# Kernel optimization log

Hardware: AMD Instinct MI355X
Metric: run time of the kernel (lower is better)

## Reference

```python
import jax, jax.numpy as jnp
import numpy as np
from jax.scipy.linalg import cho_solve

N, D, T, K, P = 4000, 256, 52, 20, 100
EPS = 1e-8


def _make_kernel(length_scale):
    # RBF kernel over time grid with the same jitter-doubling rule as the torch code.
    t = np.arange(T, dtype=np.float32)
    sq = (t[None, :] - t[:, None]) ** 2
    Kmat = np.exp(-0.5 * sq / np.float32(length_scale) ** 2).astype(np.float32)
    jitter = 1e-4
    eye = np.eye(T, dtype=np.float32)
    while True:
        if np.linalg.cond(Kmat + jitter * eye) < 1e4:
            break
        jitter *= 2
        if jitter > 0.1:
            break
    return jnp.asarray(Kmat + jitter * eye)

K_LAMBDA = _make_kernel(T / 4)  # lambda GP kernel, shared across all k
K_PHI = _make_kernel(T / 3)     # phi GP kernel, shared across all k


def setup_inputs() -> dict:
    key = jax.random.key(0)
    ks = jax.random.split(key, 7)
    lambda_ = jax.random.normal(ks[0], (N, K, T), dtype=jnp.float32)
    phi = jax.random.normal(ks[1], (K, D, T), dtype=jnp.float32)
    gamma = 0.1 * jax.random.normal(ks[2], (P, K), dtype=jnp.float32)
    G = jax.random.normal(ks[3], (N, P), dtype=jnp.float32)
    Y = (jax.random.uniform(ks[4], (N, D, T)) < 0.05).astype(jnp.float32)
    logit_prev_t = jax.random.normal(ks[5], (D, T), dtype=jnp.float32) - 3.0
    event_times = jax.random.randint(ks[6], (N, D), 0, T)
    return dict(lambda_=lambda_, phi=phi, gamma=gamma, G=G, Y=Y,
                logit_prev_t=logit_prev_t, event_times=event_times)


def reference(lambda_, phi, gamma, G, Y, logit_prev_t, event_times):
    # --- forward: softmax over topics, sigmoid disease probs, mixture ---
    theta = jax.nn.softmax(lambda_, axis=1)          # [N,K,T]
    phi_prob = jax.nn.sigmoid(phi)                   # [K,D,T]
    pi = jnp.einsum('nkt,kdt->ndt', theta, phi_prob) # [N,D,T]
    pi = jnp.clip(pi, EPS, 1.0 - EPS)

    # --- survival data loss ---
    tgrid = jnp.arange(T)[None, None, :]             # [1,1,T]
    e = event_times[:, :, None]                      # [N,D,1]
    mask_before = (tgrid < e).astype(pi.dtype)
    mask_at = (tgrid == e).astype(pi.dtype)
    log_pi = jnp.log(pi)
    log_1mpi = jnp.log1p(-pi)
    loss_censored = -jnp.sum(log_1mpi * mask_before)
    loss_event = -jnp.sum(log_pi * mask_at * Y)
    loss_no_event = -jnp.sum(log_1mpi * mask_at * (1.0 - Y))
    data_loss = (loss_censored + loss_event + loss_no_event) / N

    # --- GP prior loss: batched cholesky solves replace per-sample loops ---
    L_lam = jnp.linalg.cholesky(K_LAMBDA)            # [T,T]
    L_phi = jnp.linalg.cholesky(K_PHI)               # [T,T]
    mean_lam = G @ gamma                             # [N,K]
    dev_lam = (lambda_ - mean_lam[:, :, None]).reshape(N * K, T)  # [N*K,T]
    v_lam = cho_solve((L_lam, True), dev_lam.T)      # [T,N*K]
    gp_lambda = 0.5 * jnp.sum(dev_lam.T * v_lam)
    dev_phi = (phi - logit_prev_t[None, :, :]).reshape(K * D, T)  # [K*D,T]
    v_phi = cho_solve((L_phi, True), dev_phi.T)      # [T,K*D]
    gp_phi = 0.5 * jnp.sum(dev_phi.T * v_phi)
    gp_loss = gp_lambda / N + gp_phi / D

    return data_loss + gp_loss
```

## Files before the change

### kernel.cpp

```cpp
#include <hip/hip_runtime.h>
#include <math.h>
#include <string.h>

#define Nn 4000
#define Dd 256
#define Tt 52
#define Kk 20
#define Pp 100
#define CH 4
#define TC 13

#define OFF_W       0
#define OFF_MLAM_P  5408
#define OFF_MPHI_P  343408
#define OFF_DLP     397488
#define OFF_EVP     399488
#define OFF_PHIP    655488
#define OFF_THETA   921728

#define GR_ROWS 128

#define RB_PHIP0   0
#define RB_THETA0  52
#define RB_GPHI0   865
#define RB_GLAM0   885
#define RB_EVP0    1010
#define RB_TOTAL   1138

__global__ __launch_bounds__(256) void prep_kernel(
    const float* __restrict__ lam, const float* __restrict__ phi,
    const float* __restrict__ gamma, const float* __restrict__ G,
    const float* __restrict__ logit_prev, const int* __restrict__ ev,
    float* __restrict__ theta_t, float* __restrict__ phip_t,
    unsigned char* __restrict__ evp,
    float* __restrict__ Mlam_p, float* __restrict__ Mphi_p) {
    __shared__ float rows[GR_ROWS][56];
    __shared__ float meanv[GR_ROWS];
    const int bx = blockIdx.x, tid = threadIdx.x;

    if (bx < RB_THETA0) {
        int gid = bx * 256 + tid;
        int d = gid / Tt, t = gid - d * Tt;
        float v[Kk];
#pragma unroll
        for (int k = 0; k < Kk; ++k) {
            float x = phi[k * (Dd * Tt) + gid];
            v[k] = 1.f / (1.f + __expf(-x));
        }
#pragma unroll
        for (int k = 0; k < Kk; ++k)
            phip_t[((size_t)t * Kk + k) * Dd + d] = v[k];
        return;
    }
    if (bx < RB_GPHI0) {
        int gid = (bx - RB_THETA0) * 256 + tid;
        if (gid >= Nn * Tt) return;
        int n = gid / Tt, t = gid - n * Tt;
        const float* base = lam + n * Kk * Tt + t;
        float v[Kk];
        float m = -1e30f;
#pragma unroll
        for (int k = 0; k < Kk; ++k) { v[k] = base[k * Tt]; m = fmaxf(m, v[k]); }
        float s = 0.f;
#pragma unroll
        for (int k = 0; k < Kk; ++k) { v[k] = __expf(v[k] - m); s += v[k]; }
        float inv = 1.f / s;
        float* o = theta_t + ((size_t)t * Nn + n) * Kk;
#pragma unroll
        for (int k = 0; k < Kk; ++k) o[k] = v[k] * inv;
        return;
    }
    if (bx < RB_GLAM0) {
        int slot = bx - RB_GPHI0;
        int ta = tid % 13, tb = tid / 13;
        float acc[4][4] = {};
        for (int it = 0; it < 2; ++it) {
            int R0 = (slot * 2 + it) * GR_ROWS;
            __syncthreads();
            for (int idx = tid; idx < GR_ROWS * Tt; idx += 256) {
                int r = idx / Tt, t = idx - r * Tt;
                int R = R0 + r;
                rows[r][t] = phi[R * Tt + t] - logit_prev[(R & 255) * Tt + t];
            }
            __syncthreads();
            if (tb < 13) {
                for (int r = 0; r < GR_ROWS; ++r) {
                    float4 a = *(const float4*)&rows[r][4 * ta];
                    float4 b = *(const float4*)&rows[r][4 * tb];
                    float av[4] = {a.x, a.y, a.z, a.w};
                    float bv[4] = {b.x, b.y, b.z, b.w};
#pragma unroll
                    for (int i = 0; i < 4; ++i)
#pragma unroll
                        for (int j = 0; j < 4; ++j) acc[i][j] += av[i] * bv[j];
                }
            }
        }
        if (tb < 13)
#pragma unroll
            for (int i = 0; i < 4; ++i)
#pragma unroll
                for (int j = 0; j < 4; ++j)
                    Mphi_p[slot * 2704 + (4 * ta + i) * Tt + 4 * tb + j] = acc[i][j];
        return;
    }
    if (bx < RB_EVP0) {
        int slot = bx - RB_GLAM0;
        int ta = tid % 13, tb = tid / 13;
        float acc[4][4] = {};
        for (int it = 0; it < 5; ++it) {
            int R0 = (slot * 5 + it) * GR_ROWS;
            __syncthreads();
            if (tid < GR_ROWS) {
                int R = R0 + tid;
                int n = R / Kk, k = R - n * Kk;
                float m = 0.f;
                for (int p = 0; p < Pp; ++p) m += G[n * Pp + p] * gamma[p * Kk + k];
                meanv[tid] = m;
            }
            __syncthreads();
            for (int idx = tid; idx < GR_ROWS * Tt; idx += 256) {
                int r = idx / Tt, t = idx - r * Tt;
                int R = R0 + r;
                rows[r][t] = lam[R * Tt + t] - meanv[r];
            }
            __syncthreads();
            if (tb < 13) {
                for (int r = 0; r < GR_ROWS; ++r) {
                    float4 a = *(const float4*)&rows[r][4 * ta];
                    float4 b = *(const float4*)&rows[r][4 * tb];
                    float av[4] = {a.x, a.y, a.z, a.w};
                    float bv[4] = {b.x, b.y, b.z, b.w};
#pragma unroll
                    for (int i = 0; i < 4; ++i)
#pragma unroll
                        for (int j = 0; j < 4; ++j) acc[i][j] += av[i] * bv[j];
                }
            }
        }
        if (tb < 13)
#pragma unroll
            for (int i = 0; i < 4; ++i)
#pragma unroll
                for (int j = 0; j < 4; ++j)
                    Mlam_p[slot * 2704 + (4 * ta + i) * Tt + 4 * tb + j] = acc[i][j];
        return;
    }
    {
        const int4* src = (const int4*)ev;
        unsigned int* dst = (unsigned int*)evp;
        int gtid = (bx - RB_EVP0) * 256 + tid;
        for (int i = gtid; i < (Nn * Dd) / 4; i += 128 * 256) {
            int4 v = src[i];
            dst[i] = (unsigned)v.x | ((unsigned)v.y << 8) |
                     ((unsigned)v.z << 16) | ((unsigned)v.w << 24);
        }
        return;
    }
}

__global__ __launch_bounds__(256) void data_kernel(const float* __restrict__ theta_t,
                                                   const float* __restrict__ phip_t,
                                                   const float* __restrict__ Y,
                                                   const unsigned char* __restrict__ evp,
                                                   float* __restrict__ DLp) {
    __shared__ float wsum[4];
    const int tid = threadIdx.x;
    const int d = tid;
    const int ng = blockIdx.x >> 2;
    const int t0 = (blockIdx.x & 3) * TC;
    const int n0 = ng * 8;

    int e[8];
    float Yv[8], acc[8], pie[8], prod[8];
#pragma unroll
    for (int g = 0; g < 8; ++g) {
        e[g] = evp[(n0 + g) * Dd + d];
        acc[g] = 0.f;
        prod[g] = 1.f;
        pie[g] = 0.5f;
        Yv[g] = 0.f;
        if (e[g] >= t0 && e[g] < t0 + TC)
            Yv[g] = __builtin_nontemporal_load(
                Y + ((size_t)((n0 + g) * Dd + d)) * Tt + e[g]);
    }

    for (int j = 0; j < TC; ++j) {
        int t = t0 + j;
        float pv[Kk];
        const float* pt = phip_t + (size_t)t * (Kk * Dd) + d;
#pragma unroll
        for (int k = 0; k < Kk; ++k) pv[k] = pt[k * Dd];
#pragma unroll
        for (int g = 0; g < 8; ++g) {
            const float4* th = (const float4*)(theta_t + ((size_t)t * Nn + n0 + g) * Kk);
            float4 a0 = th[0], a1 = th[1], a2 = th[2], a3 = th[3], a4 = th[4];
            float pi = a0.x * pv[0] + a0.y * pv[1] + a0.z * pv[2] + a0.w * pv[3]
                     + a1.x * pv[4] + a1.y * pv[5] + a1.z * pv[6] + a1.w * pv[7]
                     + a2.x * pv[8] + a2.y * pv[9] + a2.z * pv[10] + a2.w * pv[11]
                     + a3.x * pv[12] + a3.y * pv[13] + a3.z * pv[14] + a3.w * pv[15]
                     + a4.x * pv[16] + a4.y * pv[17] + a4.z * pv[18] + a4.w * pv[19];
            pi = fminf(fmaxf(pi, 1e-8f), 1.0f - 1e-8f);
            prod[g] *= (t <= e[g]) ? (1.f - pi) : 1.f;
            pie[g] = (t == e[g]) ? pi : pie[g];
        }
        if ((j & 3) == 3 || j == TC - 1) {
#pragma unroll
            for (int g = 0; g < 8; ++g) { acc[g] += __logf(prod[g]); prod[g] = 1.f; }
        }
    }
    float tsum = 0.f;
#pragma unroll
    for (int g = 0; g < 8; ++g)
        tsum += acc[g] + Yv[g] * (__logf(pie[g]) - __logf(1.f - pie[g]));
    for (int off = 32; off; off >>= 1) tsum += __shfl_down(tsum, off, 64);
    if ((tid & 63) == 0) wsum[tid >> 6] = tsum;
    __syncthreads();
    if (tid == 0)
        DLp[blockIdx.x] = -(wsum[0] + wsum[1] + wsum[2] + wsum[3]);
}

__global__ __launch_bounds__(1024) void final_kernel(const float* __restrict__ ws,
                                                     float* __restrict__ out) {
    const int tid = threadIdx.x;
    double s = 0.0;
    for (int i = tid; i < 2704; i += 1024) {
        double ml = 0.0, mp = 0.0;
        for (int b = 0; b < 125; ++b) ml += (double)ws[OFF_MLAM_P + b * 2704 + i];
        for (int b = 0; b < 20; ++b)  mp += (double)ws[OFF_MPHI_P + b * 2704 + i];
        s += (double)ws[OFF_W + i] * ml + (double)ws[OFF_W + 2704 + i] * mp;
    }
    double dl = 0.0;
    for (int i = tid; i < (Nn / 8) * CH; i += 1024) dl += (double)ws[OFF_DLP + i];
    s += dl / Nn;
    __shared__ double red[1024];
    red[tid] = s;
    __syncthreads();
    for (int off = 512; off; off >>= 1) {
        if (tid < off) red[tid] += red[tid + off];
        __syncthreads();
    }
    if (tid == 0) out[0] = (float)red[0];
}


static void build_K_f(double ls_in, float Kf[52][52]) {
    float ls = (float)ls_in;
    float ls2 = ls * ls;
    for (int i = 0; i < 52; ++i)
        for (int j = 0; j < 52; ++j) {
            float sq = (float)((i - j) * (i - j));
            float arg = (-0.5f * sq) / ls2;
            Kf[i][j] = expf(arg);
        }
}

static void jacobi_eig(double a[52][52], double ev[52]) {
    const int n = 52;
    for (int sweep = 0; sweep < 100; ++sweep) {
        double off = 0;
        for (int p = 0; p < n - 1; ++p)
            for (int q = p + 1; q < n; ++q) off += a[p][q] * a[p][q];
        if (off < 1e-24) break;
        for (int p = 0; p < n - 1; ++p)
            for (int q = p + 1; q < n; ++q) {
                double apq = a[p][q];
                if (fabs(apq) < 1e-300) continue;
                double th = (a[q][q] - a[p][p]) / (2.0 * apq);
                double t = (th >= 0 ? 1.0 : -1.0) / (fabs(th) + sqrt(th * th + 1.0));
                double c = 1.0 / sqrt(t * t + 1.0), s = t * c;
                for (int i = 0; i < n; ++i) {
                    double aip = a[i][p], aiq = a[i][q];
                    a[i][p] = c * aip - s * aiq;
                    a[i][q] = s * aip + c * aiq;
                }
                for (int i = 0; i < n; ++i) {
                    double api = a[p][i], aqi = a[q][i];
                    a[p][i] = c * api - s * aqi;
                    a[q][i] = s * api + c * aqi;
                }
            }
    }
    for (int i = 0; i < n; ++i) ev[i] = a[i][i];
}

static void build_A(const float Kf[52][52], double jitter, double A[52][52]) {
    float jf = (float)jitter;
    for (int i = 0; i < 52; ++i)
        for (int j = 0; j < 52; ++j) A[i][j] = (double)Kf[i][j];
    for (int i = 0; i < 52; ++i) A[i][i] = (double)(float)(Kf[i][i] + jf);
}

static double cond_of(const float Kf[52][52], double jitter) {
    double A[52][52], ev[52];
    build_A(Kf, jitter, A);
    jacobi_eig(A, ev);
    double mx = 0.0, mn = 1e300;
    for (int i = 0; i < 52; ++i) {
        double a = fabs(ev[i]);
        if (a > mx) mx = a;
        if (a < mn) mn = a;
    }
    if (mn <= 0.0) return 1e300;
    return mx / mn;
}

static double find_jitter(const float Kf[52][52]) {
    double jitter = 1e-4;
    while (true) {
        if (cond_of(Kf, jitter) < 1e4) break;
        jitter *= 2.0;
        if (jitter > 0.1) break;
    }
    return jitter;
}

static void chol_inv_scaled(const float Kf[52][52], double jitter, double scale,
                            float* out) {
    const int n = 52;
    double A[52][52], L[52][52];
    build_A(Kf, jitter, A);
    memset(L, 0, sizeof(L));
    for (int j = 0; j < n; ++j) {
        double s = A[j][j];
        for (int k = 0; k < j; ++k) s -= L[j][k] * L[j][k];
        L[j][j] = sqrt(s);
        for (int i = j + 1; i < n; ++i) {
            double v = A[i][j];
            for (int k = 0; k < j; ++k) v -= L[i][k] * L[j][k];
            L[i][j] = v / L[j][j];
        }
    }
    for (int c = 0; c < n; ++c) {
        double y[52], x[52];
        for (int i = 0; i < n; ++i) {
            double v = (i == c) ? 1.0 : 0.0;
            for (int k = 0; k < i; ++k) v -= L[i][k] * y[k];
            y[i] = v / L[i][i];
        }
        for (int i = n - 1; i >= 0; --i) {
            double v = y[i];
            for (int k = i + 1; k < n; ++k) v -= L[k][i] * x[k];
            x[i] = v / L[i][i];
        }
        for (int i = 0; i < n; ++i) out[i * 52 + c] = (float)(x[i] * scale);
    }
}

struct KinvInit {
    float* w;
    KinvInit() {
        if (hipHostMalloc((void**)&w, 5408 * sizeof(float)) != hipSuccess)
            w = (float*)malloc(5408 * sizeof(float));
        float Kf[52][52];
        build_K_f(52.0 / 4.0, Kf);
        chol_inv_scaled(Kf, find_jitter(Kf), 0.5 / Nn, w);
        build_K_f(52.0 / 3.0, Kf);
        chol_inv_scaled(Kf, find_jitter(Kf), 0.5 / Dd, w + 2704);
    }
};
static KinvInit g_kinv;


extern "C" void kernel_launch(void* const* d_in, const int* in_sizes, int n_in,
                              void* d_out, int out_size, void* d_ws, size_t ws_size,
                              hipStream_t stream) {
    (void)in_sizes; (void)n_in; (void)out_size; (void)ws_size;
    const float* lam        = (const float*)d_in[0];
    const float* phi        = (const float*)d_in[1];
    const float* gamma      = (const float*)d_in[2];
    const float* G          = (const float*)d_in[3];
    const float* Y          = (const float*)d_in[4];
    const float* logit_prev = (const float*)d_in[5];
    const int*   ev         = (const int*)d_in[6];
    float* out = (float*)d_out;
    float* ws  = (float*)d_ws;

    hipMemcpyAsync(ws + OFF_W, g_kinv.w, 5408 * sizeof(float),
                   hipMemcpyHostToDevice, stream);

    prep_kernel<<<RB_TOTAL, 256, 0, stream>>>(
        lam, phi, gamma, G, logit_prev, ev,
        ws + OFF_THETA, ws + OFF_PHIP, (unsigned char*)(ws + OFF_EVP),
        ws + OFF_MLAM_P, ws + OFF_MPHI_P);
    data_kernel<<<(Nn / 8) * CH, 256, 0, stream>>>(
        ws + OFF_THETA, ws + OFF_PHIP, Y, (const unsigned char*)(ws + OFF_EVP),
        ws + OFF_DLP);
    final_kernel<<<1, 1024, 0, stream>>>(ws, out);
}
```

Before: 447.7 us.

## Fuse final reduction into data kernel via last-block atomic counter, repack phi/event layouts

Removes the separate final_kernel launch by having the last finishing data_kernel block, detected with an atomic counter and threadfence, do the global reduction. Event times are packed per 8-row group into a uint2 so each thread needs one load. Sigmoid(phi) is stored as float2 pairs, and the 20-term dot product is split into two partial sums. This saves one launch and some load instructions, but the single reducing block now has 256 threads instead of 1024, and the extra EVP grid blocks add work to prep.

```diff
diff --git a/kernel.cpp b/kernel.cpp
--- a/kernel.cpp
+++ b/kernel.cpp
@@ -9,14 +9,16 @@
 #define Pp 100
 #define CH 4
 #define TC 13
+#define GRID_D ((Nn / 8) * CH)
 
 #define OFF_W       0
 #define OFF_MLAM_P  5408
 #define OFF_MPHI_P  343408
 #define OFF_DLP     397488
-#define OFF_EVP     399488
-#define OFF_PHIP    655488
-#define OFF_THETA   921728
+#define OFF_CNT     399488
+#define OFF_EVP     399492
+#define OFF_PHIP2   655492
+#define OFF_THETA   921732
 
 #define GR_ROWS 128
 
@@ -25,31 +27,32 @@
 #define RB_GPHI0   865
 #define RB_GLAM0   885
 #define RB_EVP0    1010
-#define RB_TOTAL   1138
+#define RB_TOTAL   1510
 
 __global__ __launch_bounds__(256) void prep_kernel(
     const float* __restrict__ lam, const float* __restrict__ phi,
     const float* __restrict__ gamma, const float* __restrict__ G,
     const float* __restrict__ logit_prev, const int* __restrict__ ev,
-    float* __restrict__ theta_t, float* __restrict__ phip_t,
-    unsigned char* __restrict__ evp,
+    float* __restrict__ theta_t, float2* __restrict__ phip2,
+    uint2* __restrict__ evp2, unsigned int* __restrict__ cnt,
     float* __restrict__ Mlam_p, float* __restrict__ Mphi_p) {
     __shared__ float rows[GR_ROWS][56];
     __shared__ float meanv[GR_ROWS];
     const int bx = blockIdx.x, tid = threadIdx.x;
 
     if (bx < RB_THETA0) {
-        int gid = bx * 256 + tid;
-        int d = gid / Tt, t = gid - d * Tt;
+        if (bx == 0 && tid == 0) *cnt = 0u;
+        const int t = bx, d = tid;
         float v[Kk];
 #pragma unroll
         for (int k = 0; k < Kk; ++k) {
-            float x = phi[k * (Dd * Tt) + gid];
+            float x = phi[(k * Dd + d) * Tt + t];
             v[k] = 1.f / (1.f + __expf(-x));
         }
-#pragma unroll
-        for (int k = 0; k < Kk; ++k)
-            phip_t[((size_t)t * Kk + k) * Dd + d] = v[k];
+        float2* o = phip2 + (size_t)t * 10 * Dd + d;
+#pragma unroll
+        for (int kp = 0; kp < 10; ++kp)
+            o[kp * Dd] = make_float2(v[2 * kp], v[2 * kp + 1]);
         return;
     }
     if (bx < RB_GPHI0) {
@@ -147,39 +150,46 @@
         return;
     }
     {
-        const int4* src = (const int4*)ev;
-        unsigned int* dst = (unsigned int*)evp;
-        int gtid = (bx - RB_EVP0) * 256 + tid;
-        for (int i = gtid; i < (Nn * Dd) / 4; i += 128 * 256) {
-            int4 v = src[i];
-            dst[i] = (unsigned)v.x | ((unsigned)v.y << 8) |
-                     ((unsigned)v.z << 16) | ((unsigned)v.w << 24);
-        }
+        int ng = bx - RB_EVP0;
+        int n0 = ng * 8;
+        unsigned a = 0, b = 0;
+#pragma unroll
+        for (int g = 0; g < 4; ++g)
+            a |= ((unsigned)ev[(n0 + g) * Dd + tid] & 255u) << (8 * g);
+#pragma unroll
+        for (int g = 4; g < 8; ++g)
+            b |= ((unsigned)ev[(n0 + g) * Dd + tid] & 255u) << (8 * (g - 4));
+        evp2[(size_t)ng * Dd + tid] = make_uint2(a, b);
         return;
     }
 }
 
 __global__ __launch_bounds__(256) void data_kernel(const float* __restrict__ theta_t,
-                                                   const float* __restrict__ phip_t,
+                                                   const float2* __restrict__ phip2,
                                                    const float* __restrict__ Y,
-                                                   const unsigned char* __restrict__ evp,
-                                                   float* __restrict__ DLp) {
+                                                   const uint2* __restrict__ evp2,
+                                                   float* __restrict__ ws,
+                                                   float* __restrict__ out,
+                                                   unsigned int* __restrict__ cnt) {
     __shared__ float wsum[4];
+    __shared__ int isLast;
     const int tid = threadIdx.x;
     const int d = tid;
     const int ng = blockIdx.x >> 2;
     const int t0 = (blockIdx.x & 3) * TC;
     const int n0 = ng * 8;
 
+    uint2 ee = evp2[(size_t)ng * Dd + d];
     int e[8];
+    e[0] = ee.x & 255; e[1] = (ee.x >> 8) & 255;
+    e[2] = (ee.x >> 16) & 255; e[3] = (ee.x >> 24) & 255;
+    e[4] = ee.y & 255; e[5] = (ee.y >> 8) & 255;
+    e[6] = (ee.y >> 16) & 255; e[7] = (ee.y >> 24) & 255;
+
     float Yv[8], acc[8], pie[8], prod[8];
 #pragma unroll
     for (int g = 0; g < 8; ++g) {
-        e[g] = evp[(n0 + g) * Dd + d];
-        acc[g] = 0.f;
-        prod[g] = 1.f;
-        pie[g] = 0.5f;
-        Yv[g] = 0.f;
+        acc[g] = 0.f; prod[g] = 1.f; pie[g] = 0.5f; Yv[g] = 0.f;
         if (e[g] >= t0 && e[g] < t0 + TC)
             Yv[g] = __builtin_nontemporal_load(
                 Y + ((size_t)((n0 + g) * Dd + d)) * Tt + e[g]);
@@ -187,19 +197,21 @@
 
     for (int j = 0; j < TC; ++j) {
         int t = t0 + j;
-        float pv[Kk];
-        const float* pt = phip_t + (size_t)t * (Kk * Dd) + d;
-#pragma unroll
-        for (int k = 0; k < Kk; ++k) pv[k] = pt[k * Dd];
+        float2 pv[10];
+        const float2* pt = phip2 + (size_t)t * 10 * Dd + d;
+#pragma unroll
+        for (int kp = 0; kp < 10; ++kp) pv[kp] = pt[kp * Dd];
 #pragma unroll
         for (int g = 0; g < 8; ++g) {
-            const float4* th = (const float4*)(theta_t + ((size_t)t * Nn + n0 + g) * Kk);
-            float4 a0 = th[0], a1 = th[1], a2 = th[2], a3 = th[3], a4 = th[4];
-            float pi = a0.x * pv[0] + a0.y * pv[1] + a0.z * pv[2] + a0.w * pv[3]
-                     + a1.x * pv[4] + a1.y * pv[5] + a1.z * pv[6] + a1.w * pv[7]
-                     + a2.x * pv[8] + a2.y * pv[9] + a2.z * pv[10] + a2.w * pv[11]
-                     + a3.x * pv[12] + a3.y * pv[13] + a3.z * pv[14] + a3.w * pv[15]
-                     + a4.x * pv[16] + a4.y * pv[17] + a4.z * pv[18] + a4.w * pv[19];
+            const float2* th = (const float2*)(theta_t + ((size_t)t * Nn + n0 + g) * Kk);
+            float2 s2 = make_float2(0.f, 0.f);
+#pragma unroll
+            for (int kp = 0; kp < 10; ++kp) {
+                float2 a = th[kp];
+                s2.x += a.x * pv[kp].x;
+                s2.y += a.y * pv[kp].y;
+            }
+            float pi = s2.x + s2.y;
             pi = fminf(fmaxf(pi, 1e-8f), 1.0f - 1e-8f);
             prod[g] *= (t <= e[g]) ? (1.f - pi) : 1.f;
             pie[g] = (t == e[g]) ? pi : pie[g];
@@ -216,27 +228,30 @@
     for (int off = 32; off; off >>= 1) tsum += __shfl_down(tsum, off, 64);
     if ((tid & 63) == 0) wsum[tid >> 6] = tsum;
     __syncthreads();
-    if (tid == 0)
-        DLp[blockIdx.x] = -(wsum[0] + wsum[1] + wsum[2] + wsum[3]);
-}
-
-__global__ __launch_bounds__(1024) void final_kernel(const float* __restrict__ ws,
-                                                     float* __restrict__ out) {
-    const int tid = threadIdx.x;
+    if (tid == 0) {
+        ws[OFF_DLP + blockIdx.x] = -(wsum[0] + wsum[1] + wsum[2] + wsum[3]);
+        __threadfence();
+        unsigned prev = atomicAdd(cnt, 1u);
+        isLast = (prev == GRID_D - 1) ? 1 : 0;
+    }
+    __syncthreads();
+    if (!isLast) return;
+
+    __threadfence();
     double s = 0.0;
-    for (int i = tid; i < 2704; i += 1024) {
+    for (int i = tid; i < 2704; i += 256) {
         double ml = 0.0, mp = 0.0;
         for (int b = 0; b < 125; ++b) ml += (double)ws[OFF_MLAM_P + b * 2704 + i];
         for (int b = 0; b < 20; ++b)  mp += (double)ws[OFF_MPHI_P + b * 2704 + i];
         s += (double)ws[OFF_W + i] * ml + (double)ws[OFF_W + 2704 + i] * mp;
     }
     double dl = 0.0;
-    for (int i = tid; i < (Nn / 8) * CH; i += 1024) dl += (double)ws[OFF_DLP + i];
+    for (int i = tid; i < GRID_D; i += 256) dl += (double)ws[OFF_DLP + i];
     s += dl / Nn;
-    __shared__ double red[1024];
+    __shared__ double red[256];
     red[tid] = s;
     __syncthreads();
-    for (int off = 512; off; off >>= 1) {
+    for (int off = 128; off; off >>= 1) {
         if (tid < off) red[tid] += red[tid + off];
         __syncthreads();
     }
@@ -381,10 +396,10 @@
 
     prep_kernel<<<RB_TOTAL, 256, 0, stream>>>(
         lam, phi, gamma, G, logit_prev, ev,
-        ws + OFF_THETA, ws + OFF_PHIP, (unsigned char*)(ws + OFF_EVP),
+        ws + OFF_THETA, (float2*)(ws + OFF_PHIP2),
+        (uint2*)(ws + OFF_EVP), (unsigned int*)(ws + OFF_CNT),
         ws + OFF_MLAM_P, ws + OFF_MPHI_P);
-    data_kernel<<<(Nn / 8) * CH, 256, 0, stream>>>(
-        ws + OFF_THETA, ws + OFF_PHIP, Y, (const unsigned char*)(ws + OFF_EVP),
-        ws + OFF_DLP);
-    final_kernel<<<1, 1024, 0, stream>>>(ws, out);
-}
+    data_kernel<<<GRID_D, 256, 0, stream>>>(
+        ws + OFF_THETA, (const float2*)(ws + OFF_PHIP2), Y,
+        (const uint2*)(ws + OFF_EVP), ws, out, (unsigned int*)(ws + OFF_CNT));
+}
```

Result: slower. 567.4 us (+26.7%).
